# Optimization experiments

Hardware: AMD Instinct MI355X
Metric: run time of the kernel (lower is better)

Reference implementation:

```python
import jax, jax.numpy as jnp
import numpy as np
import math

# ---- static config (must match init_kwargs / input_specs) ----
D = 1024
N_HEAD = 16
HEAD_DIM = D // N_HEAD          # 64
HALF = HEAD_DIM // 2            # rope half dim = 32
N_EXP = 8
TOP_K = 2
CAP_FACTOR = 2.0
LN_EPS = 1e-5


def _build_sin_cos(T, half_dim, dtype=jnp.float32):
    pos = jnp.arange(T, dtype=dtype)[:, None]                      # (T,1)
    inv_freq = 1.0 / (10000.0 ** (jnp.arange(0, 2 * half_dim, 2, dtype=dtype) / (2 * half_dim)))
    ang = pos * inv_freq[None, :]                                  # (T, half)
    return jnp.sin(ang), jnp.cos(ang)


def _layernorm(x, g, b):
    mu = jnp.mean(x, axis=-1, keepdims=True)
    var = jnp.mean(jnp.square(x - mu), axis=-1, keepdims=True)
    return (x - mu) * jax.lax.rsqrt(var + LN_EPS) * g + b


def _apply_rope(q, k, sin, cos):
    # q,k: (B,T,H,hd); sin,cos: (T, half)
    s = sin[None, :, None, :]
    c = cos[None, :, None, :]
    q1, q2 = q[..., :HALF], q[..., HALF:]
    k1, k2 = k[..., :HALF], k[..., HALF:]
    qr = jnp.concatenate([q1 * c - q2 * s, q1 * s + q2 * c], axis=-1)
    kr = jnp.concatenate([k1 * c - k2 * s, k1 * s + k2 * c], axis=-1)
    return qr, kr


def _attention(x, Wqkv, Wproj):
    B, T, C = x.shape
    qkv = x @ Wqkv                                                  # (B,T,3C)
    qkv = qkv.reshape(B, T, N_HEAD, 3 * HEAD_DIM)
    q, k, v = jnp.split(qkv, 3, axis=-1)                            # each (B,T,H,hd)
    sin, cos = _build_sin_cos(T, HALF)
    q, k = _apply_rope(q, k, sin, cos)
    scale = 1.0 / math.sqrt(HEAD_DIM)
    att = jnp.einsum('bqhd,bkhd->bhqk', q, k) * scale               # (B,H,T,T)
    causal = jnp.tril(jnp.ones((T, T), dtype=bool))
    att = jnp.where(causal[None, None], att, jnp.finfo(att.dtype).min)
    p = jax.nn.softmax(att, axis=-1)
    o = jnp.einsum('bhqk,bkhd->bqhd', p, v).reshape(B, T, C)
    return o @ Wproj, k, v


def _sparse_moe(flat, Wgate, W1, b1, W2, b2):
    # flat: (N, d). Eval mode: no router noise.
    N, d = flat.shape
    capacity = int(math.ceil(CAP_FACTOR * N / N_EXP))
    logits = flat @ Wgate                                           # (N,E)
    gates = jax.nn.softmax(logits, axis=-1)
    vals, inds = jax.lax.top_k(gates, TOP_K)                        # (N,k)
    flat_inds = inds.reshape(-1)                                    # (N*k,)
    flat_vals = vals.reshape(-1)
    neg = jnp.finfo(flat.dtype).min
    # per-expert assignment scores over all (token, slot) pairs
    scores = jnp.where(flat_inds[None, :] == jnp.arange(N_EXP)[:, None],
                       flat_vals[None, :], neg)                     # (E, N*k)
    top_scores, top_pos = jax.lax.top_k(scores, capacity)           # (E, cap)
    tok_idx = top_pos // TOP_K                                      # (E, cap)
    w = jnp.where(top_scores > neg, top_scores, 0.0)                # dropped slots -> 0 weight
    xe = flat[tok_idx]                                              # gather: (E, cap, d)
    h = jax.nn.gelu(jnp.einsum('ecd,edh->ech', xe, W1) + b1[:, None, :], approximate=False)
    out = jnp.einsum('ech,ehd->ecd', h, W2) + b2[:, None, :]
    out = out * w[..., None]
    final = jnp.zeros_like(flat).at[tok_idx.reshape(-1)].add(out.reshape(-1, d))
    return final


def setup_inputs() -> dict:
    key = jax.random.key(0)
    ks = jax.random.split(key, 10)
    B, T = 2, 2048
    s = 0.02
    return {
        'x': jax.random.normal(ks[0], (B, T, D), dtype=jnp.float32),
        'ln1_g': jnp.ones((D,), jnp.float32),
        'ln1_b': jnp.zeros((D,), jnp.float32),
        'ln2_g': jnp.ones((D,), jnp.float32),
        'ln2_b': jnp.zeros((D,), jnp.float32),
        'Wqkv': jax.random.normal(ks[1], (D, 3 * D), jnp.float32) * s,
        'Wproj': jax.random.normal(ks[2], (D, D), jnp.float32) * s,
        'Wgate': jax.random.normal(ks[3], (D, N_EXP), jnp.float32) * s,
        'W1': jax.random.normal(ks[4], (N_EXP, D, 4 * D), jnp.float32) * s,
        'b1': jnp.zeros((N_EXP, 4 * D), jnp.float32),
        'W2': jax.random.normal(ks[5], (N_EXP, 4 * D, D), jnp.float32) * s,
        'b2': jnp.zeros((N_EXP, D), jnp.float32),
    }


def reference(x, ln1_g, ln1_b, ln2_g, ln2_b, Wqkv, Wproj, Wgate, W1, b1, W2, b2):
    B, T, _ = x.shape
    x_norm = _layernorm(x, ln1_g, ln1_b)
    attn_out, k, v = _attention(x_norm, Wqkv, Wproj)
    x = x + attn_out
    ff_in = _layernorm(x, ln2_g, ln2_b)
    moe_out = _sparse_moe(ff_in.reshape(B * T, D), Wgate, W1, b1, W2, b2)
    x = x + moe_out.reshape(B, T, D)
    aux_loss = jnp.zeros((), x.dtype)  # eval mode
    return x, aux_loss, k, v
```

## Files before the change

kernel.cpp:

```cpp
#include <hip/hip_runtime.h>
#include <hip/hip_bf16.h>
#include <math.h>


#define TT 2048
#define NTOK 4096

typedef __attribute__((ext_vector_type(8))) short bf16x8;
typedef __attribute__((ext_vector_type(4))) float f32x4;
typedef __attribute__((ext_vector_type(16))) float f32x16;

static __device__ __forceinline__ ushort f2bf(float f) {
  union { float f; unsigned u; } v; v.f = f;
  unsigned r = v.u + 0x7FFFu + ((v.u >> 16) & 1u);
  return (ushort)(r >> 16);
}
static __device__ __forceinline__ float bf2f(ushort h) {
  union { unsigned u; float f; } v; v.u = ((unsigned)h) << 16; return v.f;
}
static __device__ __forceinline__ unsigned cvt_pk_bf16(float lo, float hi) {
  unsigned r;
  asm("v_cvt_pk_bf16_f32 %0, %1, %2" : "=v"(r) : "v"(lo), "v"(hi));
  return r;
}
static __device__ __forceinline__ void plane_swap(unsigned& a, unsigned& b) {
  asm("v_permlane32_swap_b32 %0, %1" : "+v"(a), "+v"(b));
}

template<bool GATE>
__global__ __launch_bounds__(256)
void ln_kernel(const float* __restrict__ x, const float* __restrict__ g,
               const float* __restrict__ b, ushort* __restrict__ oh,
               ushort* __restrict__ ol, const float* __restrict__ Wg,
               int* __restrict__ te, float* __restrict__ tv, int* __restrict__ inv) {
  __shared__ float srow[1024];
  int row = blockIdx.x, tid = threadIdx.x;
  const float4* xr = (const float4*)(x + (size_t)row * 1024);
  float4 v = xr[tid];
  float s = v.x + v.y + v.z + v.w;
  #pragma unroll
  for (int off = 1; off < 64; off <<= 1) s += __shfl_xor(s, off);
  __shared__ float red1[4], red2[4];
  if ((tid & 63) == 0) red1[tid >> 6] = s;
  __syncthreads();
  float mu = (red1[0] + red1[1] + red1[2] + red1[3]) * (1.0f / 1024.0f);
  float dx = v.x - mu, dy = v.y - mu, dz = v.z - mu, dw = v.w - mu;
  float ss = dx*dx + dy*dy + dz*dz + dw*dw;
  #pragma unroll
  for (int off = 1; off < 64; off <<= 1) ss += __shfl_xor(ss, off);
  if ((tid & 63) == 0) red2[tid >> 6] = ss;
  __syncthreads();
  float var = (red2[0] + red2[1] + red2[2] + red2[3]) * (1.0f / 1024.0f);
  float inv_ = 1.0f / sqrtf(var + 1e-5f);
  float4 g4 = ((const float4*)g)[tid];
  float4 b4 = ((const float4*)b)[tid];
  float4 o4;
  o4.x = dx * inv_ * g4.x + b4.x;
  o4.y = dy * inv_ * g4.y + b4.y;
  o4.z = dz * inv_ * g4.z + b4.z;
  o4.w = dw * inv_ * g4.w + b4.w;
  size_t base = (size_t)row * 1024 + tid * 4;
  ushort h0 = f2bf(o4.x), h1 = f2bf(o4.y), h2 = f2bf(o4.z), h3 = f2bf(o4.w);
  ushort4 hh = {h0, h1, h2, h3};
  *(ushort4*)(oh + base) = hh;
  ushort4 ll = {f2bf(o4.x - bf2f(h0)), f2bf(o4.y - bf2f(h1)),
                f2bf(o4.z - bf2f(h2)), f2bf(o4.w - bf2f(h3))};
  *(ushort4*)(ol + base) = ll;
  if constexpr (GATE) {
    *(float4*)&srow[tid * 4] = o4;
    __syncthreads();
    float acc[8] = {};
    for (int i = tid; i < 1024; i += 256) {
      float xv = srow[i];
      const float4* wr = (const float4*)&Wg[i * 8];
      float4 w0 = wr[0], w1 = wr[1];
      acc[0] += xv * w0.x; acc[1] += xv * w0.y; acc[2] += xv * w0.z; acc[3] += xv * w0.w;
      acc[4] += xv * w1.x; acc[5] += xv * w1.y; acc[6] += xv * w1.z; acc[7] += xv * w1.w;
    }
    #pragma unroll
    for (int off = 1; off < 64; off <<= 1)
      #pragma unroll
      for (int qq = 0; qq < 8; ++qq) acc[qq] += __shfl_xor(acc[qq], off);
    __shared__ float red[4][8];
    if ((tid & 63) == 0)
      #pragma unroll
      for (int qq = 0; qq < 8; ++qq) red[tid >> 6][qq] = acc[qq];
    __syncthreads();
    if (tid == 0) {
      float gg[8];
      #pragma unroll
      for (int qq = 0; qq < 8; ++qq) gg[qq] = red[0][qq] + red[1][qq] + red[2][qq] + red[3][qq];
      float mx = gg[0];
      #pragma unroll
      for (int qq = 1; qq < 8; ++qq) mx = fmaxf(mx, gg[qq]);
      float sum = 0.0f;
      #pragma unroll
      for (int qq = 0; qq < 8; ++qq) { gg[qq] = expf(gg[qq] - mx); sum += gg[qq]; }
      float inv_s = 1.0f / sum;
      #pragma unroll
      for (int qq = 0; qq < 8; ++qq) gg[qq] *= inv_s;
      int e1 = 0; float v1 = gg[0];
      for (int qq = 1; qq < 8; ++qq) if (gg[qq] > v1) { v1 = gg[qq]; e1 = qq; }
      int e2 = -1; float v2 = -1.0f;
      for (int qq = 0; qq < 8; ++qq) { if (qq == e1) continue; if (gg[qq] > v2) { v2 = gg[qq]; e2 = qq; } }
      te[row * 2] = e1; te[row * 2 + 1] = e2;
      tv[row * 2] = v1; tv[row * 2 + 1] = v2;
      inv[row * 2] = -1; inv[row * 2 + 1] = -1;
    }
  }
}

__global__ void sincos_kernel(float* __restrict__ st, float* __restrict__ ct) {
  int t = blockIdx.x, j = threadIdx.x;
  double invf = pow(10000.0, -((double)(2 * j)) / 64.0);
  double ang = (double)t * invf;
  st[t * 32 + j] = (float)sin(ang);
  ct[t * 32 + j] = (float)cos(ang);
}

__global__ __launch_bounds__(256)
void rope_kernel(float* __restrict__ qkv, const float* __restrict__ st,
                 const float* __restrict__ ct, float* __restrict__ kout,
                 float* __restrict__ vout, ushort* __restrict__ Kh,
                 ushort* __restrict__ Kl) {
  int row = blockIdx.x;
  int t = row & (TT - 1);
  int b = row >> 11;
  int tid = threadIdx.x;
  float* base = qkv + (size_t)row * 3072;
  #pragma unroll
  for (int l = 0; l < 2; ++l) {
    int idx = l * 256 + tid;
    int h = idx >> 5, j = idx & 31;
    float s = st[t * 32 + j], c = ct[t * 32 + j];
    float* qp = base + h * 192;
    float q1 = qp[j], q2 = qp[j + 32];
    qp[j]      = q1 * c - q2 * s;
    qp[j + 32] = q1 * s + q2 * c;
    float k1 = qp[64 + j], k2 = qp[96 + j];
    float kr1 = k1 * c - k2 * s, kr2 = k1 * s + k2 * c;
    qp[64 + j] = kr1; qp[96 + j] = kr2;
    kout[(size_t)row * 1024 + h * 64 + j]      = kr1;
    kout[(size_t)row * 1024 + h * 64 + 32 + j] = kr2;
    size_t kb = ((size_t)(b * 16 + h) * TT + t) * 64;
    ushort h1 = f2bf(kr1);
    Kh[kb + j] = h1; Kl[kb + j] = f2bf(kr1 - bf2f(h1));
    ushort h2 = f2bf(kr2);
    Kh[kb + 32 + j] = h2; Kl[kb + 32 + j] = f2bf(kr2 - bf2f(h2));
  }
  #pragma unroll
  for (int l = 0; l < 4; ++l) {
    int f = l * 256 + tid;
    int h = f >> 6, d = f & 63;
    vout[(size_t)row * 1024 + f] = base[h * 192 + 128 + d];
  }
}

__global__ __launch_bounds__(256)
void vtprep_kernel(const float* __restrict__ vout, ushort* __restrict__ Vth,
                   ushort* __restrict__ Vtl) {
  __shared__ float tile[64][65];
  int t0 = blockIdx.x * 64, h = blockIdx.y, b = blockIdx.z;
  int tid = threadIdx.x;
  #pragma unroll
  for (int l = 0; l < 4; ++l) {
    int idx = l * 256 + tid;
    int r = idx >> 4, c4 = (idx & 15) * 4;
    *(float4*)&tile[r][c4] = *(const float4*)&vout[((size_t)(b * TT + t0 + r)) * 1024 + h * 64 + c4];
  }
  __syncthreads();
  int d = tid >> 2, ts = (tid & 3) * 16;
  union { bf16x8 v; ushort u[8]; } H0, H1, L0, L1;
  #pragma unroll
  for (int i = 0; i < 8; ++i) {
    float v0 = tile[ts + i][d];
    ushort hb0 = f2bf(v0);
    H0.u[i] = hb0; L0.u[i] = f2bf(v0 - bf2f(hb0));
    float v1 = tile[ts + 8 + i][d];
    ushort hb1 = f2bf(v1);
    H1.u[i] = hb1; L1.u[i] = f2bf(v1 - bf2f(hb1));
  }
  size_t basep = ((size_t)(b * 16 + h) * 64 + d) * TT + t0 + ts;
  *(bf16x8*)(Vth + basep) = H0.v;  *(bf16x8*)(Vth + basep + 8) = H1.v;
  *(bf16x8*)(Vtl + basep) = L0.v;  *(bf16x8*)(Vtl + basep + 8) = L1.v;
}

__global__ __launch_bounds__(256)
void flash8_kernel(const float* __restrict__ qkv, const ushort* __restrict__ Kh,
                   const ushort* __restrict__ Kl, const ushort* __restrict__ Vth,
                   const ushort* __restrict__ Vtl, float* __restrict__ Opart,
                   float* __restrict__ Mpart, float* __restrict__ Lpart) {
  const int offt[16] = {0,1,2,4,6,9,12,16,20,25,30,36,42,49,56,64};
  int lin = blockIdx.x;
  int xcd = lin & 7, s = lin >> 3;
  int bh = xcd + 8 * (s / 72);
  int j = 71 - (s % 72);
  int qt = 0, off = 0;
  #pragma unroll
  for (int u = 0; u < 16; ++u)
    if (j >= offt[u]) { qt = u; off = offt[u]; }
  int kc = j - off;
  int slot = bh * 72 + j;
  int h = bh & 15, b = bh >> 4;
  int tid = threadIdx.x;
  int w = tid >> 6, lane = tid & 63;
  int q = lane & 31, LH = lane >> 5;
  size_t bT = (size_t)b * TT;
  int qglob0 = qt * 128 + w * 32;
  int qg = qglob0 + q;
  bf16x8 qH[4], qL[4];
  {
    const float* qp = qkv + (bT + qg) * 3072 + h * 192 + LH * 8;
    #pragma unroll
    for (int dblk = 0; dblk < 4; ++dblk) {
      float4 f0 = *(const float4*)(qp + dblk * 16);
      float4 f1 = *(const float4*)(qp + dblk * 16 + 4);
      float vals[8] = {f0.x * 0.125f, f0.y * 0.125f, f0.z * 0.125f, f0.w * 0.125f,
                       f1.x * 0.125f, f1.y * 0.125f, f1.z * 0.125f, f1.w * 0.125f};
      union { bf16x8 v; ushort u[8]; } H, L;
      #pragma unroll
      for (int e = 0; e < 8; ++e) {
        ushort hb = f2bf(vals[e]);
        H.u[e] = hb; L.u[e] = f2bf(vals[e] - bf2f(hb));
      }
      qH[dblk] = H.v; qL[dblk] = L.v;
    }
  }
  const ushort* Kbh = Kh + (size_t)bh * TT * 64;
  const ushort* Kbl = Kl + (size_t)bh * TT * 64;
  const ushort* Vbh = Vth + (size_t)bh * 64 * TT;
  const ushort* Vbl = Vtl + (size_t)bh * 64 * TT;
  f32x16 accO0 = {}, accO1 = {};
  float m = -3.402823466e38f, lsum = 0.0f;
  int kvlo = kc * 256;
  int kvhi = min(kvlo + 256, qglob0 + 32);

  auto loadK = [&](bf16x8 (&kH)[4], bf16x8 (&kL)[4], int kv0) {
    const ushort* kbh = Kbh + (size_t)(kv0 + q) * 64 + LH * 8;
    const ushort* kbl = Kbl + (size_t)(kv0 + q) * 64 + LH * 8;
    #pragma unroll
    for (int dblk = 0; dblk < 4; ++dblk) {
      kH[dblk] = *(const bf16x8*)(kbh + dblk * 16);
      kL[dblk] = *(const bf16x8*)(kbl + dblk * 16);
    }
  };

  auto tile = [&](bf16x8 (&kH)[4], bf16x8 (&kL)[4],
                  bf16x8 (&kHn)[4], bf16x8 (&kLn)[4], int kv0, bool pf) {
    bf16x8 vAH[2][2], vAL[2][2];
    #pragma unroll
    for (int dblk = 0; dblk < 2; ++dblk)
      #pragma unroll
      for (int s2 = 0; s2 < 2; ++s2) {
        size_t ad = (size_t)(dblk * 32 + q) * TT + kv0 + s2 * 16 + LH * 8;
        vAH[dblk][s2] = *(const bf16x8*)(Vbh + ad);
        vAL[dblk][s2] = *(const bf16x8*)(Vbl + ad);
      }
    f32x16 sa = {}, sb = {};
    __builtin_amdgcn_s_setprio(1);
    sa = __builtin_amdgcn_mfma_f32_32x32x16_bf16(kH[0], qH[0], sa, 0, 0, 0);
    sb = __builtin_amdgcn_mfma_f32_32x32x16_bf16(kH[2], qH[2], sb, 0, 0, 0);
    sa = __builtin_amdgcn_mfma_f32_32x32x16_bf16(kH[1], qH[1], sa, 0, 0, 0);
    sb = __builtin_amdgcn_mfma_f32_32x32x16_bf16(kH[3], qH[3], sb, 0, 0, 0);
    sa = __builtin_amdgcn_mfma_f32_32x32x16_bf16(kH[0], qL[0], sa, 0, 0, 0);
    sb = __builtin_amdgcn_mfma_f32_32x32x16_bf16(kH[2], qL[2], sb, 0, 0, 0);
    sa = __builtin_amdgcn_mfma_f32_32x32x16_bf16(kH[1], qL[1], sa, 0, 0, 0);
    sb = __builtin_amdgcn_mfma_f32_32x32x16_bf16(kH[3], qL[3], sb, 0, 0, 0);
    sa = __builtin_amdgcn_mfma_f32_32x32x16_bf16(kL[0], qH[0], sa, 0, 0, 0);
    sb = __builtin_amdgcn_mfma_f32_32x32x16_bf16(kL[2], qH[2], sb, 0, 0, 0);
    sa = __builtin_amdgcn_mfma_f32_32x32x16_bf16(kL[1], qH[1], sa, 0, 0, 0);
    sb = __builtin_amdgcn_mfma_f32_32x32x16_bf16(kL[3], qH[3], sb, 0, 0, 0);
    __builtin_amdgcn_s_setprio(0);
    if (pf) loadK(kHn, kLn, kv0 + 32);
    float p[16];
    float pmax = -3.402823466e38f;
    if (kv0 + 31 > qglob0) {
      #pragma unroll
      for (int r = 0; r < 16; ++r) {
        int kvg = kv0 + (r & 3) + 8 * (r >> 2) + 4 * LH;
        float sv = (kvg <= qg) ? (sa[r] + sb[r]) : -3.402823466e38f;
        p[r] = sv; pmax = fmaxf(pmax, sv);
      }
    } else {
      #pragma unroll
      for (int r = 0; r < 16; ++r) {
        float sv = sa[r] + sb[r];
        p[r] = sv; pmax = fmaxf(pmax, sv);
      }
    }
    pmax = fmaxf(pmax, __shfl_xor(pmax, 32));
    float mnew = fmaxf(m, pmax);
    float fsc = __expf(m - mnew);
    float psum = 0.0f;
    #pragma unroll
    for (int r = 0; r < 16; ++r) { p[r] = __expf(p[r] - mnew); psum += p[r]; }
    psum += __shfl_xor(psum, 32);
    lsum = lsum * fsc + psum;
    m = mnew;
    #pragma unroll
    for (int r = 0; r < 16; ++r) { accO0[r] *= fsc; accO1[r] *= fsc; }
    bf16x8 pHf[2], pLf[2];
    #pragma unroll
    for (int s2 = 0; s2 < 2; ++s2) {
      int s8 = s2 * 8;
      unsigned a  = cvt_pk_bf16(p[s8 + 0], p[s8 + 1]);
      unsigned bw = cvt_pk_bf16(p[s8 + 2], p[s8 + 3]);
      unsigned c  = cvt_pk_bf16(p[s8 + 4], p[s8 + 5]);
      unsigned d  = cvt_pk_bf16(p[s8 + 6], p[s8 + 7]);
      float l0 = p[s8 + 0] - __uint_as_float(a << 16);
      float l1 = p[s8 + 1] - __uint_as_float(a & 0xFFFF0000u);
      float l2 = p[s8 + 2] - __uint_as_float(bw << 16);
      float l3 = p[s8 + 3] - __uint_as_float(bw & 0xFFFF0000u);
      float l4 = p[s8 + 4] - __uint_as_float(c << 16);
      float l5 = p[s8 + 5] - __uint_as_float(c & 0xFFFF0000u);
      float l6 = p[s8 + 6] - __uint_as_float(d << 16);
      float l7 = p[s8 + 7] - __uint_as_float(d & 0xFFFF0000u);
      unsigned al = cvt_pk_bf16(l0, l1);
      unsigned bl = cvt_pk_bf16(l2, l3);
      unsigned cl = cvt_pk_bf16(l4, l5);
      unsigned dl = cvt_pk_bf16(l6, l7);
      plane_swap(a, c); plane_swap(bw, d);
      plane_swap(al, cl); plane_swap(bl, dl);
      union { unsigned w[4]; bf16x8 v; } PH, PL;
      PH.w[0] = a;  PH.w[1] = bw; PH.w[2] = c;  PH.w[3] = d;
      PL.w[0] = al; PL.w[1] = bl; PL.w[2] = cl; PL.w[3] = dl;
      pHf[s2] = PH.v; pLf[s2] = PL.v;
    }
    __builtin_amdgcn_s_setprio(1);
    #pragma unroll
    for (int s2 = 0; s2 < 2; ++s2) {
      accO0 = __builtin_amdgcn_mfma_f32_32x32x16_bf16(vAH[0][s2], pHf[s2], accO0, 0, 0, 0);
      accO1 = __builtin_amdgcn_mfma_f32_32x32x16_bf16(vAH[1][s2], pHf[s2], accO1, 0, 0, 0);
      accO0 = __builtin_amdgcn_mfma_f32_32x32x16_bf16(vAH[0][s2], pLf[s2], accO0, 0, 0, 0);
      accO1 = __builtin_amdgcn_mfma_f32_32x32x16_bf16(vAH[1][s2], pLf[s2], accO1, 0, 0, 0);
      accO0 = __builtin_amdgcn_mfma_f32_32x32x16_bf16(vAL[0][s2], pHf[s2], accO0, 0, 0, 0);
      accO1 = __builtin_amdgcn_mfma_f32_32x32x16_bf16(vAL[1][s2], pHf[s2], accO1, 0, 0, 0);
    }
    __builtin_amdgcn_s_setprio(0);
  };

  bf16x8 kA[4], kB[4], kC[4], kD[4];
  loadK(kA, kB, kvlo);
  for (int kv0 = kvlo; kv0 < kvhi; kv0 += 64) {
    tile(kA, kB, kC, kD, kv0, kv0 + 32 < kvhi);
    if (kv0 + 32 < kvhi)
      tile(kC, kD, kA, kB, kv0 + 32, kv0 + 64 < kvhi);
  }

  if (LH == 0) {
    Mpart[slot * 128 + w * 32 + q] = m;
    Lpart[slot * 128 + w * 32 + q] = lsum;
  }
  float* Ob = Opart + (size_t)slot * 8192 + (w * 32 + q) * 64;
  #pragma unroll
  for (int g2 = 0; g2 < 4; ++g2) {
    float4 v0 = {accO0[g2 * 4 + 0], accO0[g2 * 4 + 1], accO0[g2 * 4 + 2], accO0[g2 * 4 + 3]};
    *(float4*)(Ob + 8 * g2 + 4 * LH) = v0;
    float4 v1 = {accO1[g2 * 4 + 0], accO1[g2 * 4 + 1], accO1[g2 * 4 + 2], accO1[g2 * 4 + 3]};
    *(float4*)(Ob + 32 + 8 * g2 + 4 * LH) = v1;
  }
}

__global__ __launch_bounds__(256)
void fmerge2_kernel(const float* __restrict__ Opart, const float* __restrict__ Mpart,
                    const float* __restrict__ Lpart, ushort* __restrict__ oh,
                    ushort* __restrict__ ol) {
  const int offt[16] = {0,1,2,4,6,9,12,16,20,25,30,36,42,49,56,64};
  int qt = blockIdx.x, bh = blockIdx.y;
  int h = bh & 15, b = bh >> 4;
  int nc = (qt + 2) >> 1;
  int slot0 = bh * 72 + offt[qt];
  int tid = threadIdx.x;
  int q = tid & 127, dh = tid >> 7;
  float mg = -3.402823466e38f;
  for (int c = 0; c < nc; ++c) mg = fmaxf(mg, Mpart[(slot0 + c) * 128 + q]);
  float lg = 0.0f;
  float4 acc[8] = {};
  for (int c = 0; c < nc; ++c) {
    float sc = __expf(Mpart[(slot0 + c) * 128 + q] - mg);
    lg += sc * Lpart[(slot0 + c) * 128 + q];
    const float4* op = (const float4*)(Opart + (size_t)(slot0 + c) * 8192 + q * 64 + dh * 32);
    #pragma unroll
    for (int i = 0; i < 8; ++i) {
      float4 v = op[i];
      acc[i].x += sc * v.x; acc[i].y += sc * v.y;
      acc[i].z += sc * v.z; acc[i].w += sc * v.w;
    }
  }
  float inv = 1.0f / lg;
  size_t obase = ((size_t)(b * TT + qt * 128 + q)) * 1024 + h * 64 + dh * 32;
  #pragma unroll
  for (int i = 0; i < 8; ++i) {
    float4 v = {acc[i].x * inv, acc[i].y * inv, acc[i].z * inv, acc[i].w * inv};
    ushort h0 = f2bf(v.x), h1 = f2bf(v.y), h2 = f2bf(v.z), h3 = f2bf(v.w);
    ushort4 hh = {h0, h1, h2, h3};
    *(ushort4*)(oh + obase + i * 4) = hh;
    ushort4 ll = {f2bf(v.x - bf2f(h0)), f2bf(v.y - bf2f(h1)),
                  f2bf(v.z - bf2f(h2)), f2bf(v.w - bf2f(h3))};
    *(ushort4*)(ol + obase + i * 4) = ll;
  }
}

template<bool LO>
__global__ void tconv_kernel(const float* __restrict__ in, ushort* __restrict__ oh,
                             ushort* __restrict__ ol, int K, int N) {
  __shared__ float t[32][33];
  int z = blockIdx.z;
  const float* ip = in + (size_t)z * K * N;
  ushort* ohp = oh + (size_t)z * K * N;
  ushort* olp = LO ? (ol + (size_t)z * K * N) : nullptr;
  int n0 = blockIdx.x * 32, k0 = blockIdx.y * 32;
  int tx = threadIdx.x, ty = threadIdx.y;
  #pragma unroll
  for (int i = 0; i < 4; ++i)
    t[ty + 8 * i][tx] = ip[(size_t)(k0 + ty + 8 * i) * N + n0 + tx];
  __syncthreads();
  #pragma unroll
  for (int i = 0; i < 4; ++i) {
    float v = t[tx][ty + 8 * i];
    size_t off = (size_t)(n0 + ty + 8 * i) * K + k0 + tx;
    ushort hb = f2bf(v);
    ohp[off] = hb;
    if (LO) olp[off] = f2bf(v - bf2f(hb));
  }
}

#define LOAD_STEP(tt) do {                                                     \
    int seg = SPLIT3 ? ((tt) / kPer) : 0;                                      \
    int kk = (SPLIT3 ? ((tt) % kPer) : (tt)) << 6;                             \
    const ushort* Ause = (SPLIT3 && seg == 2) ? AlB : AhB;                     \
    const ushort* Buse = (SPLIT3 && seg == 1) ? BlB : BhB;                     \
    _Pragma("unroll")                                                          \
    for (int q = 0; q < 4; ++q) {                                              \
      int rr = r0 + 32 * q;                                                    \
      int clog = cph ^ (rr & 7);                                               \
      ra[q] = *(const bf16x8*)(Ause + (size_t)garow[q] * K + kk + clog * 8);   \
      rb[q] = *(const bf16x8*)(Buse + (size_t)(bn + rr) * K + kk + clog * 8);  \
    }                                                                          \
  } while (0)

template<int EPI, bool GATHER, bool SPLIT3>
__global__ __launch_bounds__(256, 2)
void mgemm(const ushort* __restrict__ Ah, const ushort* __restrict__ Al,
           const ushort* __restrict__ Bh, const ushort* __restrict__ Bl,
           void* __restrict__ Cv, const float* __restrict__ extra,
           const int* __restrict__ gatAll, int N, int K,
           long aEStride, long bEStride, long cEStride, int biasEStride) {
  __shared__ ushort As[128 * 64];
  __shared__ ushort Bs[128 * 64];
  int z = blockIdx.z;
  const ushort* AhB = Ah + (size_t)z * aEStride;
  const ushort* AlB = SPLIT3 ? (Al + (size_t)z * aEStride) : nullptr;
  const ushort* BhB = Bh + (size_t)z * bEStride;
  const ushort* BlB = SPLIT3 ? (Bl + (size_t)z * bEStride) : nullptr;
  const int* gat = GATHER ? (gatAll + z * 1024) : nullptr;
  int bm = blockIdx.y * 128, bn = blockIdx.x * 128;
  int tid = threadIdx.x;
  int r0 = tid >> 3, cph = tid & 7;
  int garow[4];
  #pragma unroll
  for (int q = 0; q < 4; ++q) {
    int rr = r0 + 32 * q;
    garow[q] = GATHER ? gat[bm + rr] : (bm + rr);
  }
  int kPer = K >> 6;
  int kSteps = (SPLIT3 ? 3 : 1) * kPer;
  int wid = tid >> 6, lane = tid & 63;
  int wm = wid >> 1, wn = wid & 1;
  int lr = lane & 15, lk = lane >> 4;
  f32x4 acc[4][4] = {};
  bf16x8 ra[4], rb[4];
  LOAD_STEP(0);
  for (int t = 0; t < kSteps; ++t) {
    __syncthreads();
    #pragma unroll
    for (int q = 0; q < 4; ++q) {
      int rr = r0 + 32 * q;
      *(bf16x8*)&As[rr * 64 + cph * 8] = ra[q];
      *(bf16x8*)&Bs[rr * 64 + cph * 8] = rb[q];
    }
    __syncthreads();
    if (t + 1 < kSteps) LOAD_STEP(t + 1);
    #pragma unroll
    for (int kh = 0; kh < 2; ++kh) {
      bf16x8 af[4], bfr[4];
      #pragma unroll
      for (int mf = 0; mf < 4; ++mf) {
        int row = wm * 64 + mf * 16 + lr;
        int ch = (kh * 4 + lk) ^ (row & 7);
        af[mf] = *(const bf16x8*)&As[row * 64 + ch * 8];
      }
      #pragma unroll
      for (int nf = 0; nf < 4; ++nf) {
        int row = wn * 64 + nf * 16 + lr;
        int ch = (kh * 4 + lk) ^ (row & 7);
        bfr[nf] = *(const bf16x8*)&Bs[row * 64 + ch * 8];
      }
      #pragma unroll
      for (int mf = 0; mf < 4; ++mf)
        #pragma unroll
        for (int nf = 0; nf < 4; ++nf)
          acc[mf][nf] = __builtin_amdgcn_mfma_f32_16x16x32_bf16(af[mf], bfr[nf], acc[mf][nf], 0, 0, 0);
    }
  }
  int crow = bm + wm * 64, ccol = bn + wn * 64;
  if constexpr (EPI <= 1) {
    float* C = (float*)Cv;
    #pragma unroll
    for (int mf = 0; mf < 4; ++mf)
      #pragma unroll
      for (int nf = 0; nf < 4; ++nf)
        #pragma unroll
        for (int r = 0; r < 4; ++r) {
          int row = crow + mf * 16 + lk * 4 + r;
          int col = ccol + nf * 16 + lr;
          float v = acc[mf][nf][r];
          if constexpr (EPI == 1) v += extra[(size_t)row * N + col];
          C[(size_t)row * N + col] = v;
        }
  } else {
    const float* bias = extra + (size_t)z * biasEStride;
    ushort* C = (ushort*)Cv + (size_t)z * cEStride;
    #pragma unroll
    for (int mf = 0; mf < 4; ++mf)
      #pragma unroll
      for (int nf = 0; nf < 4; ++nf)
        #pragma unroll
        for (int r = 0; r < 4; ++r) {
          int row = crow + mf * 16 + lk * 4 + r;
          int col = ccol + nf * 16 + lr;
          float v = acc[mf][nf][r] + bias[col];
          if constexpr (EPI == 2)
            v = 0.5f * v * (1.0f + erff(v * 0.70710678118654752f));
          C[(size_t)row * N + col] = f2bf(v);
        }
  }
}

__global__ __launch_bounds__(1024)
void route_sort_kernel(const int* __restrict__ te, const float* __restrict__ tv,
                       int* __restrict__ etok, float* __restrict__ ew,
                       int* __restrict__ inv) {
  __shared__ unsigned long long sk[4096];
  __shared__ int wcnt[16];
  __shared__ int base;
  int e = blockIdx.x, tid = threadIdx.x;
  int lane = tid & 63, wv = tid >> 6;
  if (tid == 0) base = 0;
  __syncthreads();
  for (int c = 0; c < 8; ++c) {
    int s = c * 1024 + tid;
    bool sel = (te[s] == e);
    unsigned long long ball = __ballot(sel);
    int pre = __popcll(ball & ((1ull << lane) - 1ull));
    if (lane == 0) wcnt[wv] = __popcll(ball);
    __syncthreads();
    int woff = 0, tot = 0;
    #pragma unroll
    for (int i = 0; i < 16; ++i) {
      int cc = wcnt[i];
      if (i < wv) woff += cc;
      tot += cc;
    }
    if (sel) {
      unsigned vb = __float_as_uint(tv[s]);
      sk[base + woff + pre] =
          ((unsigned long long)vb << 32) | (unsigned)(0xFFFFFFFFu - (unsigned)s);
    }
    __syncthreads();
    if (tid == 0) base += tot;
    __syncthreads();
  }
  int n = base;
  if (n > 1024) {
    int P = (n <= 2048) ? 2048 : 4096;
    for (int i = n + tid; i < P; i += 1024) sk[i] = 0ull;
    __syncthreads();
    for (int k = 2; k <= P; k <<= 1)
      for (int j = k >> 1; j > 0; j >>= 1) {
        for (int t = tid; t < (P >> 1); t += 1024) {
          int i = ((t & ~(j - 1)) << 1) | (t & (j - 1));
          int p = i | j;
          unsigned long long a = sk[i], bq = sk[p];
          bool desc = ((i & k) == 0);
          if (desc ? (a < bq) : (a > bq)) { sk[i] = bq; sk[p] = a; }
        }
        __syncthreads();
      }
  }
  int cap = n < 1024 ? n : 1024;
  if (tid < cap) {
    unsigned long long key = sk[tid];
    unsigned slot = 0xFFFFFFFFu - (unsigned)(key & 0xFFFFFFFFull);
    etok[e * 1024 + tid] = (int)(slot >> 1);
    ew[e * 1024 + tid] = __uint_as_float((unsigned)(key >> 32));
    inv[slot] = e * 1024 + tid;
  } else {
    etok[e * 1024 + tid] = 0;
    ew[e * 1024 + tid] = 0.0f;
  }
}

__global__ __launch_bounds__(256)
void combine_kernel(const float* __restrict__ xres, const ushort* __restrict__ eo,
                    const int* __restrict__ inv, const float* __restrict__ ew,
                    float* __restrict__ outx, float* __restrict__ aux) {
  int token = blockIdx.x;
  int d = threadIdx.x * 4;
  float4 acc = *(const float4*)&xres[(size_t)token * 1024 + d];
  #pragma unroll
  for (int j = 0; j < 2; ++j) {
    int p = inv[token * 2 + j];
    if (p >= 0) {
      float w = ew[p];
      const ushort* ep = eo + (size_t)p * 1024 + d;
      acc.x += w * bf2f(ep[0]); acc.y += w * bf2f(ep[1]);
      acc.z += w * bf2f(ep[2]); acc.w += w * bf2f(ep[3]);
    }
  }
  *(float4*)&outx[(size_t)token * 1024 + d] = acc;
  if (token == 0 && threadIdx.x == 0) aux[0] = 0.0f;
}

extern "C" void kernel_launch(void* const* d_in, const int* in_sizes, int n_in,
                              void* d_out, int out_size, void* d_ws, size_t ws_size,
                              hipStream_t stream) {
  const float* x     = (const float*)d_in[0];
  const float* ln1g  = (const float*)d_in[1];
  const float* ln1b  = (const float*)d_in[2];
  const float* ln2g  = (const float*)d_in[3];
  const float* ln2b  = (const float*)d_in[4];
  const float* Wqkv  = (const float*)d_in[5];
  const float* Wproj = (const float*)d_in[6];
  const float* Wg    = (const float*)d_in[7];
  const float* W1    = (const float*)d_in[8];
  const float* b1    = (const float*)d_in[9];
  const float* W2    = (const float*)d_in[10];
  const float* b2    = (const float*)d_in[11];

  float* out_x   = (float*)d_out;
  float* out_aux = out_x + 4194304;
  float* out_k   = out_aux + 1;
  float* out_v   = out_k + 4194304;

  float* ws   = (float*)d_ws;
  float* A    = ws;
  float* qkvb = ws + 4194304;
  float* st   = ws + 20971520;
  float* ct   = ws + 21037056;
  int*   te   = (int*)(ws + 21102592);
  float* tv   = ws + 21110784;
  int*   etok = (int*)(ws + 21118976);
  float* ew   = ws + 21127168;
  int*   inv  = (int*)(ws + 21135360);
  ushort* bfAh = (ushort*)(ws + 21143552);
  ushort* bfAl = (ushort*)(ws + 23240704);
  ushort* BqH  = (ushort*)(ws + 25337856);
  ushort* BqL  = (ushort*)(ws + 26910720);
  ushort* BpH  = (ushort*)(ws + 28483584);
  ushort* BpL  = (ushort*)(ws + 29007872);
  ushort* W1t  = (ushort*)(ws + 29532160);
  ushort* W2t  = (ushort*)(ws + 46309376);
  ushort* eo   = (ushort*)(ws + 63086592);
  ushort* hbuf = (ushort*)(ws + 4194304);
  ushort* Kh_  = bfAh;
  ushort* Kl_  = bfAl;
  ushort* Vth_ = eo;
  ushort* Vtl_ = eo + 4194304;
  float* Opart = ws + 29532160;
  float* Mpart = ws + 48406528;
  float* Lpart = ws + 48701440;

  tconv_kernel<true ><<<dim3(96, 32, 1),  dim3(32, 8), 0, stream>>>(Wqkv,  BqH, BqL, 1024, 3072);
  tconv_kernel<true ><<<dim3(32, 32, 1),  dim3(32, 8), 0, stream>>>(Wproj, BpH, BpL, 1024, 1024);
  sincos_kernel<<<TT, 32, 0, stream>>>(st, ct);

  ln_kernel<false><<<NTOK, 256, 0, stream>>>(x, ln1g, ln1b, bfAh, bfAl,
                                             nullptr, nullptr, nullptr, nullptr);
  mgemm<0, false, true><<<dim3(24, 32, 1), 256, 0, stream>>>(
      bfAh, bfAl, BqH, BqL, qkvb, nullptr, nullptr, 3072, 1024, 0, 0, 0, 0);
  rope_kernel<<<NTOK, 256, 0, stream>>>(qkvb, st, ct, out_k, out_v, Kh_, Kl_);
  vtprep_kernel<<<dim3(32, 16, 2), 256, 0, stream>>>(out_v, Vth_, Vtl_);
  flash8_kernel<<<2304, 256, 0, stream>>>(qkvb, Kh_, Kl_, Vth_, Vtl_, Opart, Mpart, Lpart);
  fmerge2_kernel<<<dim3(16, 32), 256, 0, stream>>>(Opart, Mpart, Lpart, bfAh, bfAl);
  mgemm<1, false, true><<<dim3(8, 32, 1), 256, 0, stream>>>(
      bfAh, bfAl, BpH, BpL, A, x, nullptr, 1024, 1024, 0, 0, 0, 0);
  tconv_kernel<false><<<dim3(128, 32, 8), dim3(32, 8), 0, stream>>>(W1, W1t, nullptr, 1024, 4096);
  tconv_kernel<false><<<dim3(32, 128, 8), dim3(32, 8), 0, stream>>>(W2, W2t, nullptr, 4096, 1024);
  ln_kernel<true><<<NTOK, 256, 0, stream>>>(A, ln2g, ln2b, bfAh, bfAl, Wg, te, tv, inv);
  route_sort_kernel<<<8, 1024, 0, stream>>>(te, tv, etok, ew, inv);
  mgemm<2, true, false><<<dim3(32, 8, 8), 256, 0, stream>>>(
      bfAh, nullptr, W1t, nullptr, hbuf, b1, etok, 4096, 1024,
      0, 4096L * 1024, 1024L * 4096, 4096);
  mgemm<3, false, false><<<dim3(8, 8, 8), 256, 0, stream>>>(
      hbuf, nullptr, W2t, nullptr, eo, b2, nullptr, 1024, 4096,
      1024L * 4096, 1024L * 4096, 1024L * 1024, 1024);
  combine_kernel<<<NTOK, 256, 0, stream>>>(A, eo, inv, ew, out_x, out_aux);
}
```

Before: 694.9 us.

## Widen flash KV chunks to 512, use exp2 softmax, and XCD-remap GEMM tiles

The flash attention split-KV chunk grows from 256 to 512 keys, which cuts the work items from 72 to 40 per batch-head. That means fewer partial outputs to write and merge, and the slot mapping in the merge kernel changes to match. Q is prescaled by log2(e) so the softmax can use the raw v_exp_f32 instruction in place of __expf. The mgemm kernel also remaps workgroup IDs so that neighbouring tiles land on the same XCD, for better L2 reuse. The price is less parallelism in flash, with 1280 blocks instead of 2304, and possibly worse load balance.

```diff
diff --git a/kernel.cpp b/kernel.cpp
--- a/kernel.cpp
+++ b/kernel.cpp
@@ -25,6 +25,11 @@
 }
 static __device__ __forceinline__ void plane_swap(unsigned& a, unsigned& b) {
   asm("v_permlane32_swap_b32 %0, %1" : "+v"(a), "+v"(b));
+}
+static __device__ __forceinline__ float fexp2(float x) {
+  float r;
+  asm("v_exp_f32 %0, %1" : "=v"(r) : "v"(x));
+  return r;
 }
 
 template<bool GATE>
@@ -186,21 +191,20 @@
 }
 
 __global__ __launch_bounds__(256)
-void flash8_kernel(const float* __restrict__ qkv, const ushort* __restrict__ Kh,
+void flash9_kernel(const float* __restrict__ qkv, const ushort* __restrict__ Kh,
                    const ushort* __restrict__ Kl, const ushort* __restrict__ Vth,
                    const ushort* __restrict__ Vtl, float* __restrict__ Opart,
                    float* __restrict__ Mpart, float* __restrict__ Lpart) {
-  const int offt[16] = {0,1,2,4,6,9,12,16,20,25,30,36,42,49,56,64};
   int lin = blockIdx.x;
   int xcd = lin & 7, s = lin >> 3;
-  int bh = xcd + 8 * (s / 72);
-  int j = 71 - (s % 72);
-  int qt = 0, off = 0;
-  #pragma unroll
-  for (int u = 0; u < 16; ++u)
-    if (j >= offt[u]) { qt = u; off = offt[u]; }
-  int kc = j - off;
-  int slot = bh * 72 + j;
+  int bh = xcd + 8 * (s / 40);
+  int j = 39 - (s % 40);
+  int qt, kc;
+  if (j < 4)       { qt = j;                    kc = 0; }
+  else if (j < 12) { qt = 4 + ((j - 4) >> 1);   kc = (j - 4) & 1; }
+  else if (j < 24) { qt = 8 + (j - 12) / 3;     kc = (j - 12) % 3; }
+  else             { qt = 12 + ((j - 24) >> 2); kc = (j - 24) & 3; }
+  int slot = bh * 40 + j;
   int h = bh & 15, b = bh >> 4;
   int tid = threadIdx.x;
   int w = tid >> 6, lane = tid & 63;
@@ -210,13 +214,14 @@
   int qg = qglob0 + q;
   bf16x8 qH[4], qL[4];
   {
+    const float qs = 0.125f * 1.44269504088896340736f;
     const float* qp = qkv + (bT + qg) * 3072 + h * 192 + LH * 8;
     #pragma unroll
     for (int dblk = 0; dblk < 4; ++dblk) {
       float4 f0 = *(const float4*)(qp + dblk * 16);
       float4 f1 = *(const float4*)(qp + dblk * 16 + 4);
-      float vals[8] = {f0.x * 0.125f, f0.y * 0.125f, f0.z * 0.125f, f0.w * 0.125f,
-                       f1.x * 0.125f, f1.y * 0.125f, f1.z * 0.125f, f1.w * 0.125f};
+      float vals[8] = {f0.x * qs, f0.y * qs, f0.z * qs, f0.w * qs,
+                       f1.x * qs, f1.y * qs, f1.z * qs, f1.w * qs};
       union { bf16x8 v; ushort u[8]; } H, L;
       #pragma unroll
       for (int e = 0; e < 8; ++e) {
@@ -232,8 +237,8 @@
   const ushort* Vbl = Vtl + (size_t)bh * 64 * TT;
   f32x16 accO0 = {}, accO1 = {};
   float m = -3.402823466e38f, lsum = 0.0f;
-  int kvlo = kc * 256;
-  int kvhi = min(kvlo + 256, qglob0 + 32);
+  int kvlo = kc * 512;
+  int kvhi = min(kvlo + 512, qglob0 + 32);
 
   auto loadK = [&](bf16x8 (&kH)[4], bf16x8 (&kL)[4], int kv0) {
     const ushort* kbh = Kbh + (size_t)(kv0 + q) * 64 + LH * 8;
@@ -290,10 +295,10 @@
     }
     pmax = fmaxf(pmax, __shfl_xor(pmax, 32));
     float mnew = fmaxf(m, pmax);
-    float fsc = __expf(m - mnew);
+    float fsc = fexp2(m - mnew);
     float psum = 0.0f;
     #pragma unroll
-    for (int r = 0; r < 16; ++r) { p[r] = __expf(p[r] - mnew); psum += p[r]; }
+    for (int r = 0; r < 16; ++r) { p[r] = fexp2(p[r] - mnew); psum += p[r]; }
     psum += __shfl_xor(psum, 32);
     lsum = lsum * fsc + psum;
     m = mnew;
@@ -365,11 +370,12 @@
 void fmerge2_kernel(const float* __restrict__ Opart, const float* __restrict__ Mpart,
                     const float* __restrict__ Lpart, ushort* __restrict__ oh,
                     ushort* __restrict__ ol) {
-  const int offt[16] = {0,1,2,4,6,9,12,16,20,25,30,36,42,49,56,64};
   int qt = blockIdx.x, bh = blockIdx.y;
   int h = bh & 15, b = bh >> 4;
-  int nc = (qt + 2) >> 1;
-  int slot0 = bh * 72 + offt[qt];
+  int g = qt >> 2;
+  int nc = g + 1;
+  int off = 2 * g * (g + 1) + (qt & 3) * (g + 1);
+  int slot0 = bh * 40 + off;
   int tid = threadIdx.x;
   int q = tid & 127, dh = tid >> 7;
   float mg = -3.402823466e38f;
@@ -377,7 +383,7 @@
   float lg = 0.0f;
   float4 acc[8] = {};
   for (int c = 0; c < nc; ++c) {
-    float sc = __expf(Mpart[(slot0 + c) * 128 + q] - mg);
+    float sc = fexp2(Mpart[(slot0 + c) * 128 + q] - mg);
     lg += sc * Lpart[(slot0 + c) * 128 + q];
     const float4* op = (const float4*)(Opart + (size_t)(slot0 + c) * 8192 + q * 64 + dh * 32);
     #pragma unroll
@@ -454,7 +460,18 @@
   const ushort* BhB = Bh + (size_t)z * bEStride;
   const ushort* BlB = SPLIT3 ? (Bl + (size_t)z * bEStride) : nullptr;
   const int* gat = GATHER ? (gatAll + z * 1024) : nullptr;
-  int bm = blockIdx.y * 128, bn = blockIdx.x * 128;
+  int bx = blockIdx.x, by = blockIdx.y;
+  {
+    int nwg = gridDim.x * gridDim.y;
+    if ((nwg & 7) == 0) {
+      int lid = bx + by * gridDim.x;
+      int cpx = nwg >> 3;
+      int wgid = (lid & 7) * cpx + (lid >> 3);
+      bx = wgid % gridDim.x;
+      by = wgid / gridDim.x;
+    }
+  }
+  int bm = by * 128, bn = bx * 128;
   int tid = threadIdx.x;
   int r0 = tid >> 3, cph = tid & 7;
   int garow[4];
@@ -668,8 +685,8 @@
   ushort* Vth_ = eo;
   ushort* Vtl_ = eo + 4194304;
   float* Opart = ws + 29532160;
-  float* Mpart = ws + 48406528;
-  float* Lpart = ws + 48701440;
+  float* Mpart = ws + 40017920;
+  float* Lpart = ws + 40181760;
 
   tconv_kernel<true ><<<dim3(96, 32, 1),  dim3(32, 8), 0, stream>>>(Wqkv,  BqH, BqL, 1024, 3072);
   tconv_kernel<true ><<<dim3(32, 32, 1),  dim3(32, 8), 0, stream>>>(Wproj, BpH, BpL, 1024, 1024);
@@ -681,7 +698,7 @@
       bfAh, bfAl, BqH, BqL, qkvb, nullptr, nullptr, 3072, 1024, 0, 0, 0, 0);
   rope_kernel<<<NTOK, 256, 0, stream>>>(qkvb, st, ct, out_k, out_v, Kh_, Kl_);
   vtprep_kernel<<<dim3(32, 16, 2), 256, 0, stream>>>(out_v, Vth_, Vtl_);
-  flash8_kernel<<<2304, 256, 0, stream>>>(qkvb, Kh_, Kl_, Vth_, Vtl_, Opart, Mpart, Lpart);
+  flash9_kernel<<<1280, 256, 0, stream>>>(qkvb, Kh_, Kl_, Vth_, Vtl_, Opart, Mpart, Lpart);
   fmerge2_kernel<<<dim3(16, 32), 256, 0, stream>>>(Opart, Mpart, Lpart, bfAh, bfAl);
   mgemm<1, false, true><<<dim3(8, 32, 1), 256, 0, stream>>>(
       bfAh, bfAl, BpH, BpL, A, x, nullptr, 1024, 1024, 0, 0, 0, 0);
```

After: 689.2 us. Within noise of the previous version (-0.8%).
